# Kernel optimization log

Measured on AMD Instinct MI355X. Metric: run time of the kernel, lower is better.

The kernel has to match this reference:

```python
import jax, jax.numpy as jnp
import numpy as np

N0 = 16384; F_IN = 384; H = 512; E0 = 131072
DEPTH = 2; RATIO = 0.25; START_K = 6; K_INC = 1; INTERP_K = 6


def _pdist2(a, b):
    # squared euclidean distances [Na, Nb]
    d2 = jnp.sum(a * a, axis=1)[:, None] + jnp.sum(b * b, axis=1)[None, :] - 2.0 * (a @ b.T)
    return jnp.maximum(d2, 0.0)


def _fps(pos, n_keep):
    # farthest point sampling, deterministic start at node 0
    sel0 = jnp.zeros((n_keep,), jnp.int32)
    dist0 = jnp.sum((pos - pos[0]) ** 2, axis=-1)

    def body(i, st):
        sel, dist = st
        idx = jnp.argmax(dist).astype(jnp.int32)
        sel = sel.at[i].set(idx)
        dist = jnp.minimum(dist, jnp.sum((pos - pos[idx]) ** 2, axis=-1))
        return (sel, dist)

    sel, _ = jax.lax.fori_loop(1, n_keep, body, (sel0, dist0))
    return sel


def _knn_graph(pos, k):
    n = pos.shape[0]
    d2 = _pdist2(pos, pos)
    d2 = d2.at[jnp.arange(n), jnp.arange(n)].set(1e10)  # exclude self
    _, nbr = jax.lax.top_k(-d2, k)                      # [n, k] nearest neighbors
    src = nbr.reshape(-1)                               # flow: source_to_target
    dst = jnp.repeat(jnp.arange(n, dtype=nbr.dtype), k)
    return src, dst


def _gcn(x, src, dst, W, b):
    # GCNConv(improved=True): A_hat = D^-1/2 (A + 2I) D^-1/2, edge weights = 1
    n = x.shape[0]
    h = x @ W
    deg = jax.ops.segment_sum(jnp.ones(src.shape[0], x.dtype), dst, num_segments=n) + 2.0
    dinv = jax.lax.rsqrt(deg)
    coef = dinv[src] * dinv[dst]
    agg = jax.ops.segment_sum(h[src] * coef[:, None], dst, num_segments=n)
    agg = agg + h * (2.0 * dinv * dinv)[:, None]        # self loops with weight 2
    return agg + b


def _knn_interpolate(x, pos_x, pos_y, k):
    # interpolate coarse features x at pos_x onto fine positions pos_y (PyG knn_interpolate)
    d2 = _pdist2(pos_y, pos_x)                          # [Ny, Nx]
    negd, idx = jax.lax.top_k(-d2, k)                   # k nearest coarse points
    w = 1.0 / jnp.maximum(-negd, 1e-16)                 # [Ny, k]
    num = jnp.einsum('yk,ykf->yf', w, x[idx])
    return num / jnp.sum(w, axis=-1, keepdims=True)


def setup_inputs() -> dict:
    key = jax.random.key(0)
    ks = jax.random.split(key, 16)
    def w(k, fin, fout):
        return (jax.random.normal(k, (fin, fout), jnp.float32) / np.sqrt(fin)).astype(jnp.float32)
    return {
        'x': jax.random.normal(ks[0], (N0, F_IN), jnp.float32),
        'pos': jax.random.uniform(ks[1], (N0, 2), jnp.float32) * 100.0,
        'edge_index': jax.random.randint(ks[2], (2, E0), 0, N0, dtype=jnp.int32),
        'W_down0': w(ks[3], F_IN, H), 'b_down0': jnp.zeros((H,), jnp.float32),
        'W_down1': w(ks[4], H, H),   'b_down1': jnp.zeros((H,), jnp.float32),
        'W_up0': w(ks[5], H, H),     'b_up0': jnp.zeros((H,), jnp.float32),
        'W_up1': w(ks[6], H, H),     'b_up1': jnp.zeros((H,), jnp.float32),
        'W_lin': w(ks[7], H, H),     'b_lin': jnp.zeros((H,), jnp.float32),
    }


def reference(x, pos, edge_index, W_down0, b_down0, W_down1, b_down1,
              W_up0, b_up0, W_up1, b_up1, W_lin, b_lin):
    src, dst = edge_index[0], edge_index[1]
    Wd = [(W_down0, b_down0), (W_down1, b_down1)]
    Wu = [(W_up0, b_up0), (W_up1, b_up1)]
    all_pos = [pos]
    all_edges = [(src, dst)]
    for i in range(DEPTH):
        x = jax.nn.relu(_gcn(x, src, dst, *Wd[i]))
        n_keep = int(x.shape[0] * RATIO)
        perm = _fps(jax.lax.stop_gradient(pos), n_keep)
        pos = pos[perm]
        src, dst = _knn_graph(pos, START_K + i * K_INC)
        x = x[perm]
        all_pos.append(pos)
        all_edges.append((src, dst))
    for i in range(DEPTH):
        x = _knn_interpolate(x, all_pos[-i - 1], all_pos[-i - 2], INTERP_K)
        s, d = all_edges[-i - 2]
        x = jax.nn.relu(_gcn(x, s, d, *Wu[i]))
    return x @ W_lin + b_lin
```

## Files before the change

### kernel.cpp

```cpp
#include <hip/hip_runtime.h>

#define N0 16384
#define N1 4096
#define N2 1024
#define E0C 131072
#define FIN 384
#define HF 512

__device__ inline float4 f4fma(float w, const float4 v, float4 a) {
  a.x = fmaf(w, v.x, a.x); a.y = fmaf(w, v.y, a.y);
  a.z = fmaf(w, v.z, a.z); a.w = fmaf(w, v.w, a.w);
  return a;
}

__global__ __launch_bounds__(256)
void count_deg(const int* __restrict__ dst, int* __restrict__ cnt, int E) {
  int e = blockIdx.x * 256 + threadIdx.x;
  if (e < E) atomicAdd(&cnt[dst[e]], 1);
}

__global__ __launch_bounds__(1024)
void scan_offsets(const int* __restrict__ cnt, int* __restrict__ offs,
                  float* __restrict__ dinv) {
  __shared__ int ts[1024];
  const int t = threadIdx.x;
  int local[16];
  int sum = 0;
  #pragma unroll
  for (int j = 0; j < 16; ++j) { local[j] = cnt[t * 16 + j]; sum += local[j]; }
  ts[t] = sum;
  __syncthreads();
  for (int off = 1; off < 1024; off <<= 1) {
    int v = (t >= off) ? ts[t - off] : 0;
    __syncthreads();
    ts[t] += v;
    __syncthreads();
  }
  int run = ts[t] - sum;
  #pragma unroll
  for (int j = 0; j < 16; ++j) {
    offs[t * 16 + j] = run;
    dinv[t * 16 + j] = 1.0f / sqrtf((float)local[j] + 2.0f);
    run += local[j];
  }
  if (t == 1023) offs[N0] = run;
}

__global__ __launch_bounds__(256)
void fill_csr(const int* __restrict__ src, const int* __restrict__ dst,
              const int* __restrict__ offs, int* __restrict__ cursor,
              int* __restrict__ srcl, int E) {
  int e = blockIdx.x * 256 + threadIdx.x;
  if (e < E) {
    int d = dst[e];
    int p = atomicAdd(&cursor[d], 1);
    srcl[offs[d] + p] = src[e];
  }
}

template<int BM, int BN, int BK>
__global__ __launch_bounds__(256)
void gemm_f32(const float* __restrict__ A, const float* __restrict__ W,
              const float* __restrict__ bias, float* __restrict__ C,
              int M, int N, int K, int addBias) {
  __shared__ float As[BK][BM + 4];
  __shared__ float Ws[BK][BN];
  const int tid = threadIdx.x;
  const int bm = blockIdx.x * BM;
  const int bn = blockIdx.y * BN;
  const int tx = tid & 15;
  const int ty = tid >> 4;
  float acc[8][4];
  #pragma unroll
  for (int i = 0; i < 8; ++i)
    #pragma unroll
    for (int j = 0; j < 4; ++j) acc[i][j] = 0.f;

  for (int k0 = 0; k0 < K; k0 += BK) {
    #pragma unroll
    for (int h = 0; h < (BM * BK) / (256 * 4); ++h) {
      int q = tid + h * 256;
      int r = q >> 2;
      int c = (q & 3) << 2;
      float4 v = *(const float4*)(A + (size_t)(bm + r) * K + k0 + c);
      As[c][r] = v.x; As[c + 1][r] = v.y; As[c + 2][r] = v.z; As[c + 3][r] = v.w;
    }
    {
      int kk = tid >> 4;
      int n = (tid & 15) << 2;
      *(float4*)(&Ws[kk][n]) = *(const float4*)(W + (size_t)(k0 + kk) * N + bn + n);
    }
    __syncthreads();
    #pragma unroll
    for (int kk = 0; kk < BK; ++kk) {
      float4 b4 = *(const float4*)(&Ws[kk][tx << 2]);
      float4 a0 = *(const float4*)(&As[kk][ty << 3]);
      float4 a1 = *(const float4*)(&As[kk][(ty << 3) + 4]);
      float a[8] = {a0.x, a0.y, a0.z, a0.w, a1.x, a1.y, a1.z, a1.w};
      float b[4] = {b4.x, b4.y, b4.z, b4.w};
      #pragma unroll
      for (int i = 0; i < 8; ++i)
        #pragma unroll
        for (int j = 0; j < 4; ++j)
          acc[i][j] = fmaf(a[i], b[j], acc[i][j]);
    }
    __syncthreads();
  }
  #pragma unroll
  for (int i = 0; i < 8; ++i) {
    int row = bm + (ty << 3) + i;
    float4 o = {acc[i][0], acc[i][1], acc[i][2], acc[i][3]};
    if (addBias) {
      const float4 bb = *(const float4*)(bias + bn + (tx << 2));
      o.x += bb.x; o.y += bb.y; o.z += bb.z; o.w += bb.w;
    }
    *(float4*)(C + (size_t)row * N + bn + (tx << 2)) = o;
  }
}

__global__ __launch_bounds__(256)
void gcn_agg_csr(const float* __restrict__ h, const int* __restrict__ offs,
                 const int* __restrict__ srcl, const float* __restrict__ dinv,
                 const float* __restrict__ bias, float* __restrict__ out, int n) {
  const int wid = threadIdx.x >> 6, lane = threadIdx.x & 63;
  const int node = blockIdx.x * 4 + wid;
  if (node >= n) return;
  const float di = dinv[node];
  const int s0 = offs[node], s1 = offs[node + 1];
  float4 a0 = {0, 0, 0, 0}, a1 = {0, 0, 0, 0};
  for (int e = s0; e < s1; ++e) {
    const int s = srcl[e];
    const float w = dinv[s] * di;
    const float4* r = (const float4*)(h + (size_t)s * HF);
    a0 = f4fma(w, r[lane], a0);
    a1 = f4fma(w, r[64 + lane], a1);
  }
  const float sw = 2.0f * di * di;
  const float4* rs = (const float4*)(h + (size_t)node * HF);
  a0 = f4fma(sw, rs[lane], a0);
  a1 = f4fma(sw, rs[64 + lane], a1);
  const float4 b0 = *(const float4*)(bias + (lane << 2));
  const float4 b1 = *(const float4*)(bias + 256 + (lane << 2));
  a0.x = fmaxf(a0.x + b0.x, 0.f); a0.y = fmaxf(a0.y + b0.y, 0.f);
  a0.z = fmaxf(a0.z + b0.z, 0.f); a0.w = fmaxf(a0.w + b0.w, 0.f);
  a1.x = fmaxf(a1.x + b1.x, 0.f); a1.y = fmaxf(a1.y + b1.y, 0.f);
  a1.z = fmaxf(a1.z + b1.z, 0.f); a1.w = fmaxf(a1.w + b1.w, 0.f);
  float4* o = (float4*)(out + (size_t)node * HF);
  o[lane] = a0; o[64 + lane] = a1;
}

template<int K>
__global__ __launch_bounds__(256)
void gcn_agg_knn(const float* __restrict__ h, const int* __restrict__ nbr,
                 const float* __restrict__ bias, float* __restrict__ out, int n) {
  const int wid = threadIdx.x >> 6, lane = threadIdx.x & 63;
  const int node = blockIdx.x * 4 + wid;
  if (node >= n) return;
  const float di = 1.0f / sqrtf((float)(K + 2));
  const float w = di * di;
  float4 a0 = {0, 0, 0, 0}, a1 = {0, 0, 0, 0};
  #pragma unroll
  for (int j = 0; j < K; ++j) {
    const int s = nbr[node * K + j];
    const float4* r = (const float4*)(h + (size_t)s * HF);
    a0 = f4fma(w, r[lane], a0);
    a1 = f4fma(w, r[64 + lane], a1);
  }
  const float sw = 2.0f * di * di;
  const float4* rs = (const float4*)(h + (size_t)node * HF);
  a0 = f4fma(sw, rs[lane], a0);
  a1 = f4fma(sw, rs[64 + lane], a1);
  const float4 b0 = *(const float4*)(bias + (lane << 2));
  const float4 b1 = *(const float4*)(bias + 256 + (lane << 2));
  a0.x = fmaxf(a0.x + b0.x, 0.f); a0.y = fmaxf(a0.y + b0.y, 0.f);
  a0.z = fmaxf(a0.z + b0.z, 0.f); a0.w = fmaxf(a0.w + b0.w, 0.f);
  a1.x = fmaxf(a1.x + b1.x, 0.f); a1.y = fmaxf(a1.y + b1.y, 0.f);
  a1.z = fmaxf(a1.z + b1.z, 0.f); a1.w = fmaxf(a1.w + b1.w, 0.f);
  float4* o = (float4*)(out + (size_t)node * HF);
  o[lane] = a0; o[64 + lane] = a1;
}

__global__ __launch_bounds__(256)
void bin_hist(const float* __restrict__ pos, int* __restrict__ cid,
              int* __restrict__ hist, int n) {
  int i = blockIdx.x * 256 + threadIdx.x;
  if (i >= n) return;
  float x = pos[2 * i], y = pos[2 * i + 1];
  int cxi = (int)(x * 0.32f); cxi = cxi < 0 ? 0 : (cxi > 31 ? 31 : cxi);
  int cyi = (int)(y * 0.32f); cyi = cyi < 0 ? 0 : (cyi > 31 ? 31 : cyi);
  int c = cyi * 32 + cxi;
  cid[i] = c;
  atomicAdd(&hist[c], 1);
}

__global__ __launch_bounds__(1024)
void bin_scan(const int* __restrict__ hist, int* __restrict__ offs) {
  __shared__ int ts[1024];
  const int t = threadIdx.x;
  int v = hist[t];
  ts[t] = v;
  __syncthreads();
  for (int off = 1; off < 1024; off <<= 1) {
    int u = (t >= off) ? ts[t - off] : 0;
    __syncthreads();
    ts[t] += u;
    __syncthreads();
  }
  offs[t] = ts[t] - v;
  if (t == 1023) offs[1024] = ts[t];
}

__global__ __launch_bounds__(256)
void bin_scatter(const float* __restrict__ pos, const int* __restrict__ cid,
                 const int* __restrict__ offs, int* __restrict__ cursor,
                 float* __restrict__ sx, float* __restrict__ sy,
                 int* __restrict__ sid, int n) {
  int i = blockIdx.x * 256 + threadIdx.x;
  if (i >= n) return;
  int c = cid[i];
  int p = atomicAdd(&cursor[c], 1);
  int slot = offs[c] + p;
  sx[slot] = pos[2 * i];
  sy[slot] = pos[2 * i + 1];
  sid[slot] = i;
}

template<int NN>
__device__ __forceinline__ unsigned ror16(unsigned v) {
  return (unsigned)__builtin_amdgcn_update_dpp(0, (int)v, 0x120 | NN, 0xF, 0xF, false);
}

__device__ __forceinline__ void comb(unsigned& hi, unsigned& lo, float& x, float& y,
                                     unsigned ohi, unsigned olo, float ox, float oy) {
  unsigned long long a = ((unsigned long long)hi << 32) | lo;
  unsigned long long b = ((unsigned long long)ohi << 32) | olo;
  if (b > a) { hi = ohi; lo = olo; x = ox; y = oy; }
}

template<int N, int CHUNK, int NKEEP>
__global__ __launch_bounds__(1024)
void fps_pruned(const float* __restrict__ pos0,
                const float* __restrict__ sx, const float* __restrict__ sy,
                const int* __restrict__ sid,
                int* __restrict__ perm, float* __restrict__ pos_out) {
  const int t = threadIdx.x;
  const int base = t * CHUNK;
  float px[CHUNK], py[CHUNK], d[CHUNK];
  int id[CHUNK];
  float xmn = 3.4e38f, xmx = -3.4e38f, ymn = 3.4e38f, ymx = -3.4e38f;
  #pragma unroll
  for (int j = 0; j < CHUNK; ++j) {
    px[j] = sx[base + j]; py[j] = sy[base + j]; id[j] = sid[base + j];
    xmn = fminf(xmn, px[j]); xmx = fmaxf(xmx, px[j]);
    ymn = fminf(ymn, py[j]); ymx = fmaxf(ymx, py[j]);
  }
  float cx = pos0[0], cy = pos0[1];
  if (t == 0) { perm[0] = 0; pos_out[0] = cx; pos_out[1] = cy; }

  unsigned chi = 0, clo = 0; float ccx = 0.f, ccy = 0.f;
  {
    unsigned long long best = 0;
    #pragma unroll
    for (int j = 0; j < CHUNK; ++j) {
      float dx = __fsub_rn(px[j], cx), dy = __fsub_rn(py[j], cy);
      float nd = __fadd_rn(__fmul_rn(dx, dx), __fmul_rn(dy, dy));
      d[j] = nd;
      unsigned long long kv = ((unsigned long long)__float_as_uint(nd) << 32) |
                              (unsigned)(~(unsigned)id[j]);
      if (kv > best) { best = kv; ccx = px[j]; ccy = py[j]; }
    }
    chi = (unsigned)(best >> 32); clo = (unsigned)best;
  }
  float cmaxv = __uint_as_float(chi);

  __shared__ float4 e1[64];
  __shared__ float bc[2];

  for (int i = 1; i < NKEEP; ++i) {
    unsigned hi = chi, lo = clo; float wx = ccx, wy = ccy;
    {
      unsigned ohi, olo, ox, oy;
      ohi = ror16<1>(hi); olo = ror16<1>(lo); ox = ror16<1>(__float_as_uint(wx)); oy = ror16<1>(__float_as_uint(wy));
      comb(hi, lo, wx, wy, ohi, olo, __uint_as_float(ox), __uint_as_float(oy));
      ohi = ror16<2>(hi); olo = ror16<2>(lo); ox = ror16<2>(__float_as_uint(wx)); oy = ror16<2>(__float_as_uint(wy));
      comb(hi, lo, wx, wy, ohi, olo, __uint_as_float(ox), __uint_as_float(oy));
      ohi = ror16<4>(hi); olo = ror16<4>(lo); ox = ror16<4>(__float_as_uint(wx)); oy = ror16<4>(__float_as_uint(wy));
      comb(hi, lo, wx, wy, ohi, olo, __uint_as_float(ox), __uint_as_float(oy));
      ohi = ror16<8>(hi); olo = ror16<8>(lo); ox = ror16<8>(__float_as_uint(wx)); oy = ror16<8>(__float_as_uint(wy));
      comb(hi, lo, wx, wy, ohi, olo, __uint_as_float(ox), __uint_as_float(oy));
    }
    if ((t & 15) == 0)
      e1[t >> 4] = make_float4(__uint_as_float(hi), __uint_as_float(lo), wx, wy);
    __syncthreads();
    if (t < 16) {
      float4 a = e1[t];
      unsigned fhi = __float_as_uint(a.x), flo = __float_as_uint(a.y);
      float fx = a.z, fy = a.w;
      float4 b = e1[t + 16];
      comb(fhi, flo, fx, fy, __float_as_uint(b.x), __float_as_uint(b.y), b.z, b.w);
      b = e1[t + 32];
      comb(fhi, flo, fx, fy, __float_as_uint(b.x), __float_as_uint(b.y), b.z, b.w);
      b = e1[t + 48];
      comb(fhi, flo, fx, fy, __float_as_uint(b.x), __float_as_uint(b.y), b.z, b.w);
      unsigned ohi, olo, ox, oy;
      ohi = ror16<1>(fhi); olo = ror16<1>(flo); ox = ror16<1>(__float_as_uint(fx)); oy = ror16<1>(__float_as_uint(fy));
      comb(fhi, flo, fx, fy, ohi, olo, __uint_as_float(ox), __uint_as_float(oy));
      ohi = ror16<2>(fhi); olo = ror16<2>(flo); ox = ror16<2>(__float_as_uint(fx)); oy = ror16<2>(__float_as_uint(fy));
      comb(fhi, flo, fx, fy, ohi, olo, __uint_as_float(ox), __uint_as_float(oy));
      ohi = ror16<4>(fhi); olo = ror16<4>(flo); ox = ror16<4>(__float_as_uint(fx)); oy = ror16<4>(__float_as_uint(fy));
      comb(fhi, flo, fx, fy, ohi, olo, __uint_as_float(ox), __uint_as_float(oy));
      ohi = ror16<8>(fhi); olo = ror16<8>(flo); ox = ror16<8>(__float_as_uint(fx)); oy = ror16<8>(__float_as_uint(fy));
      comb(fhi, flo, fx, fy, ohi, olo, __uint_as_float(ox), __uint_as_float(oy));
      if (t == 0) {
        int idx = (int)(~flo);
        perm[i] = idx;
        pos_out[2 * i] = fx; pos_out[2 * i + 1] = fy;
        bc[0] = fx; bc[1] = fy;
      }
    }
    __syncthreads();
    cx = bc[0]; cy = bc[1];

    float mdx = fmaxf(fmaxf(__fsub_rn(xmn, cx), __fsub_rn(cx, xmx)), 0.f);
    float mdy = fmaxf(fmaxf(__fsub_rn(ymn, cy), __fsub_rn(cy, ymx)), 0.f);
    float mb = mdx * mdx + mdy * mdy;
    if (!(mb * 0.99999f > cmaxv)) {
      unsigned long long best = 0;
      float nccx = 0.f, nccy = 0.f;
      #pragma unroll
      for (int j = 0; j < CHUNK; ++j) {
        float dx = __fsub_rn(px[j], cx), dy = __fsub_rn(py[j], cy);
        float nd = __fadd_rn(__fmul_rn(dx, dx), __fmul_rn(dy, dy));
        float dn = fminf(d[j], nd);
        d[j] = dn;
        unsigned long long kv = ((unsigned long long)__float_as_uint(dn) << 32) |
                                (unsigned)(~(unsigned)id[j]);
        if (kv > best) { best = kv; nccx = px[j]; nccy = py[j]; }
      }
      chi = (unsigned)(best >> 32); clo = (unsigned)best;
      ccx = nccx; ccy = nccy;
      cmaxv = __uint_as_float(chi);
    }
  }
}

__global__ __launch_bounds__(256)
void gather_rows(const float* __restrict__ xin, const int* __restrict__ perm,
                 float* __restrict__ xout, int n) {
  const int wid = threadIdx.x >> 6, lane = threadIdx.x & 63;
  const int i = blockIdx.x * 4 + wid;
  if (i >= n) return;
  const int s = perm[i];
  const float4* r = (const float4*)(xin + (size_t)s * HF);
  float4* o = (float4*)(xout + (size_t)i * HF);
  o[lane] = r[lane];
  o[64 + lane] = r[64 + lane];
}

template<int NPTS, int K>
__global__ __launch_bounds__(256)
void knn_graph_kernel(const float* __restrict__ pos, int* __restrict__ srcout) {
  __shared__ float sx[NPTS], sy[NPTS], ss[NPTS];
  const int tid = threadIdx.x;
  for (int idx = tid; idx < NPTS; idx += 256) {
    float x = pos[2 * idx], y = pos[2 * idx + 1];
    sx[idx] = x; sy[idx] = y;
    ss[idx] = __fadd_rn(__fmul_rn(x, x), __fmul_rn(y, y));
  }
  __syncthreads();
  const int q = blockIdx.x * 256 + tid;
  const float qx = sx[q], qy = sy[q], qs = ss[q];
  float bd[K]; int bi[K];
  #pragma unroll
  for (int m = 0; m < K; ++m) { bd[m] = 3.4e38f; bi[m] = 0; }
  for (int j = 0; j < NPTS; ++j) {
    if (j == q) continue;
    float dot = __fadd_rn(__fmul_rn(qx, sx[j]), __fmul_rn(qy, sy[j]));
    float d2 = fmaxf(__fsub_rn(__fadd_rn(qs, ss[j]), __fmul_rn(2.0f, dot)), 0.0f);
    if (d2 < bd[K - 1]) {
      bool pr[K];
      #pragma unroll
      for (int m = 0; m < K; ++m) pr[m] = (d2 < bd[m]);
      #pragma unroll
      for (int m = K - 1; m >= 1; --m) {
        bd[m] = pr[m] ? (pr[m - 1] ? bd[m - 1] : d2) : bd[m];
        bi[m] = pr[m] ? (pr[m - 1] ? bi[m - 1] : j) : bi[m];
      }
      if (pr[0]) { bd[0] = d2; bi[0] = j; }
    }
  }
  #pragma unroll
  for (int m = 0; m < K; ++m) srcout[q * K + m] = bi[m];
}

template<int NX, int K>
__global__ __launch_bounds__(256)
void interp_topk(const float* __restrict__ posy, const float* __restrict__ posx,
                 int* __restrict__ oidx, float* __restrict__ ow,
                 float* __restrict__ owsum) {
  __shared__ float sx[NX], sy[NX], ss[NX];
  const int tid = threadIdx.x;
  for (int idx = tid; idx < NX; idx += 256) {
    float x = posx[2 * idx], y = posx[2 * idx + 1];
    sx[idx] = x; sy[idx] = y;
    ss[idx] = __fadd_rn(__fmul_rn(x, x), __fmul_rn(y, y));
  }
  __syncthreads();
  const int q = blockIdx.x * 256 + tid;
  const float qx = posy[2 * q], qy = posy[2 * q + 1];
  const float qs = __fadd_rn(__fmul_rn(qx, qx), __fmul_rn(qy, qy));
  float bd[K]; int bi[K];
  #pragma unroll
  for (int m = 0; m < K; ++m) { bd[m] = 3.4e38f; bi[m] = 0; }
  for (int j = 0; j < NX; ++j) {
    float dot = __fadd_rn(__fmul_rn(qx, sx[j]), __fmul_rn(qy, sy[j]));
    float d2 = fmaxf(__fsub_rn(__fadd_rn(qs, ss[j]), __fmul_rn(2.0f, dot)), 0.0f);
    if (d2 < bd[K - 1]) {
      bool pr[K];
      #pragma unroll
      for (int m = 0; m < K; ++m) pr[m] = (d2 < bd[m]);
      #pragma unroll
      for (int m = K - 1; m >= 1; --m) {
        bd[m] = pr[m] ? (pr[m - 1] ? bd[m - 1] : d2) : bd[m];
        bi[m] = pr[m] ? (pr[m - 1] ? bi[m - 1] : j) : bi[m];
      }
      if (pr[0]) { bd[0] = d2; bi[0] = j; }
    }
  }
  float wsum = 0.f;
  #pragma unroll
  for (int m = 0; m < K; ++m) {
    float w = 1.0f / fmaxf(bd[m], 1e-16f);
    ow[q * K + m] = w;
    oidx[q * K + m] = bi[m];
    wsum = __fadd_rn(wsum, w);
  }
  owsum[q] = wsum;
}

template<int K>
__global__ __launch_bounds__(256)
void interp_combine(const float* __restrict__ xin, const int* __restrict__ idx,
                    const float* __restrict__ w, const float* __restrict__ wsum,
                    float* __restrict__ out, int ny) {
  const int wid = threadIdx.x >> 6, lane = threadIdx.x & 63;
  const int q = blockIdx.x * 4 + wid;
  if (q >= ny) return;
  float4 a0 = {0, 0, 0, 0}, a1 = {0, 0, 0, 0};
  #pragma unroll
  for (int m = 0; m < K; ++m) {
    const int s = idx[q * K + m];
    const float wk = w[q * K + m];
    const float4* r = (const float4*)(xin + (size_t)s * HF);
    a0 = f4fma(wk, r[lane], a0);
    a1 = f4fma(wk, r[64 + lane], a1);
  }
  const float inv = wsum[q];
  a0.x /= inv; a0.y /= inv; a0.z /= inv; a0.w /= inv;
  a1.x /= inv; a1.y /= inv; a1.z /= inv; a1.w /= inv;
  float4* o = (float4*)(out + (size_t)q * HF);
  o[lane] = a0; o[64 + lane] = a1;
}

extern "C" void kernel_launch(void* const* d_in, const int* in_sizes, int n_in,
                              void* d_out, int out_size, void* d_ws, size_t ws_size,
                              hipStream_t stream) {
  const float* x    = (const float*)d_in[0];
  const float* pos  = (const float*)d_in[1];
  const int*   ei   = (const int*)d_in[2];
  const float* Wd0  = (const float*)d_in[3];
  const float* bd0  = (const float*)d_in[4];
  const float* Wd1  = (const float*)d_in[5];
  const float* bd1  = (const float*)d_in[6];
  const float* Wu0  = (const float*)d_in[7];
  const float* bu0  = (const float*)d_in[8];
  const float* Wu1  = (const float*)d_in[9];
  const float* bu1  = (const float*)d_in[10];
  const float* Wl   = (const float*)d_in[11];
  const float* bl   = (const float*)d_in[12];
  float* out = (float*)d_out;

  char* ws = (char*)d_ws;
  size_t off = 0;
  auto alloc = [&](size_t bytes) -> char* {
    char* p = ws + off;
    off = (off + bytes + 255) & ~(size_t)255;
    return p;
  };
  float* bufA   = (float*)alloc((size_t)N0 * HF * 4);
  float* bufB   = (float*)alloc((size_t)N0 * HF * 4);
  float* bufC   = (float*)alloc((size_t)N1 * HF * 4);
  float* x2     = (float*)alloc((size_t)N2 * HF * 4);
  int*   offs0  = (int*)alloc((N0 + 1) * 4);
  int*   srcl0  = (int*)alloc(E0C * 4);
  int*   cnt    = (int*)alloc(N0 * 4);
  int*   cursor = (int*)alloc(N0 * 4);
  float* dinv0  = (float*)alloc(N0 * 4);
  int*   perm0  = (int*)alloc(N1 * 4);
  float* pos1   = (float*)alloc(N1 * 2 * 4);
  int*   src1   = (int*)alloc(N1 * 6 * 4);
  int*   perm1  = (int*)alloc(N2 * 4);
  float* pos2   = (float*)alloc(N2 * 2 * 4);
  int*   iidx   = (int*)alloc((size_t)N0 * 6 * 4);
  float* iw     = (float*)alloc((size_t)N0 * 6 * 4);
  float* iwsum  = (float*)alloc(N0 * 4);
  float* bsx    = (float*)alloc(N0 * 4);
  float* bsy    = (float*)alloc(N0 * 4);
  int*   bsid   = (int*)alloc(N0 * 4);
  int*   bcid   = (int*)alloc(N0 * 4);
  int*   bhist  = (int*)alloc(1024 * 4);
  int*   bcur   = (int*)alloc(1024 * 4);
  int*   boffs  = (int*)alloc(1025 * 4);

  float* h1   = bufB;
  float* x1f  = bufB + (size_t)N1 * HF;
  float* hu0  = bufB;
  float* xu0f = bufB + (size_t)N1 * HF;

  hipMemsetAsync(cnt, 0, N0 * 4, stream);
  hipMemsetAsync(cursor, 0, N0 * 4, stream);
  count_deg<<<E0C / 256, 256, 0, stream>>>(ei + E0C, cnt, E0C);
  scan_offsets<<<1, 1024, 0, stream>>>(cnt, offs0, dinv0);
  fill_csr<<<E0C / 256, 256, 0, stream>>>(ei, ei + E0C, offs0, cursor, srcl0, E0C);

  hipMemsetAsync(bhist, 0, 1024 * 4, stream);
  hipMemsetAsync(bcur, 0, 1024 * 4, stream);
  bin_hist<<<N0 / 256, 256, 0, stream>>>(pos, bcid, bhist, N0);
  bin_scan<<<1, 1024, 0, stream>>>(bhist, boffs);
  bin_scatter<<<N0 / 256, 256, 0, stream>>>(pos, bcid, boffs, bcur, bsx, bsy, bsid, N0);

  gemm_f32<128, 64, 16><<<dim3(N0 / 128, HF / 64), 256, 0, stream>>>(
      x, Wd0, nullptr, bufA, N0, HF, FIN, 0);
  gcn_agg_csr<<<N0 / 4, 256, 0, stream>>>(bufA, offs0, srcl0, dinv0, bd0, bufB, N0);
  fps_pruned<N0, 16, N1><<<1, 1024, 0, stream>>>(pos, bsx, bsy, bsid, perm0, pos1);
  gather_rows<<<N1 / 4, 256, 0, stream>>>(bufB, perm0, bufC, N1);
  knn_graph_kernel<N1, 6><<<N1 / 256, 256, 0, stream>>>(pos1, src1);

  hipMemsetAsync(bhist, 0, 1024 * 4, stream);
  hipMemsetAsync(bcur, 0, 1024 * 4, stream);
  bin_hist<<<N1 / 256, 256, 0, stream>>>(pos1, bcid, bhist, N1);
  bin_scan<<<1, 1024, 0, stream>>>(bhist, boffs);
  bin_scatter<<<N1 / 256, 256, 0, stream>>>(pos1, bcid, boffs, bcur, bsx, bsy, bsid, N1);

  gemm_f32<128, 64, 16><<<dim3(N1 / 128, HF / 64), 256, 0, stream>>>(
      bufC, Wd1, nullptr, h1, N1, HF, HF, 0);
  gcn_agg_knn<6><<<N1 / 4, 256, 0, stream>>>(h1, src1, bd1, x1f, N1);
  fps_pruned<N1, 4, N2><<<1, 1024, 0, stream>>>(pos1, bsx, bsy, bsid, perm1, pos2);
  gather_rows<<<N2 / 4, 256, 0, stream>>>(x1f, perm1, x2, N2);

  interp_topk<N2, 6><<<N1 / 256, 256, 0, stream>>>(pos1, pos2, iidx, iw, iwsum);
  interp_combine<6><<<N1 / 4, 256, 0, stream>>>(x2, iidx, iw, iwsum, bufC, N1);
  gemm_f32<128, 64, 16><<<dim3(N1 / 128, HF / 64), 256, 0, stream>>>(
      bufC, Wu0, nullptr, hu0, N1, HF, HF, 0);
  gcn_agg_knn<6><<<N1 / 4, 256, 0, stream>>>(hu0, src1, bu0, xu0f, N1);

  interp_topk<N1, 6><<<N0 / 256, 256, 0, stream>>>(pos, pos1, iidx, iw, iwsum);
  interp_combine<6><<<N0 / 4, 256, 0, stream>>>(xu0f, iidx, iw, iwsum, bufA, N0);
  gemm_f32<128, 64, 16><<<dim3(N0 / 128, HF / 64), 256, 0, stream>>>(
      bufA, Wu1, nullptr, bufB, N0, HF, HF, 0);
  gcn_agg_csr<<<N0 / 4, 256, 0, stream>>>(bufB, offs0, srcl0, dinv0, bu1, bufA, N0);

  gemm_f32<128, 64, 16><<<dim3(N0 / 128, HF / 64), 256, 0, stream>>>(
      bufA, Wl, bl, out, N0, HF, HF, 1);
}
```

Baseline: 9.219 ms.

## Restructure FPS argmax reduction to single-wave pass with positions in LDS

Rewrites the farthest-point-sampling kernel so each thread publishes its chunk's best key to shared memory. A single wave then reduces all candidates with a strided scan, DPP row rotations and readlanes, instead of every thread running a DPP reduction followed by a second cross-row stage. Point coordinates move from registers into shared memory to lower register pressure. The second FPS level now runs with 256 threads instead of 1024. This trims per-iteration reduction work on the serial critical path, at the cost of a shared-memory read per point in the distance update and a serial scan over 16 candidates per lane in the 1024-thread case.

```diff
diff --git a/kernel.cpp b/kernel.cpp
--- a/kernel.cpp
+++ b/kernel.cpp
@@ -230,92 +230,95 @@
   return (unsigned)__builtin_amdgcn_update_dpp(0, (int)v, 0x120 | NN, 0xF, 0xF, false);
 }
 
-__device__ __forceinline__ void comb(unsigned& hi, unsigned& lo, float& x, float& y,
-                                     unsigned ohi, unsigned olo, float ox, float oy) {
-  unsigned long long a = ((unsigned long long)hi << 32) | lo;
-  unsigned long long b = ((unsigned long long)ohi << 32) | olo;
-  if (b > a) { hi = ohi; lo = olo; x = ox; y = oy; }
-}
-
-template<int N, int CHUNK, int NKEEP>
-__global__ __launch_bounds__(1024)
-void fps_pruned(const float* __restrict__ pos0,
-                const float* __restrict__ sx, const float* __restrict__ sy,
-                const int* __restrict__ sid,
-                int* __restrict__ perm, float* __restrict__ pos_out) {
+template<int N, int NCH, int NKEEP>
+__global__ __launch_bounds__(NCH)
+void fps_fast(const float* __restrict__ pos0,
+              const float* __restrict__ sx, const float* __restrict__ sy,
+              const int* __restrict__ sid,
+              int* __restrict__ perm, float* __restrict__ pos_out) {
+  constexpr int CHUNK = N / NCH;
   const int t = threadIdx.x;
   const int base = t * CHUNK;
-  float px[CHUNK], py[CHUNK], d[CHUNK];
-  int id[CHUNK];
+
+  __shared__ float pxl[N];
+  __shared__ float pyl[N];
+  __shared__ unsigned long long ck[NCH];
+  __shared__ float2 cp[NCH];
+  __shared__ float bc[2];
+
+  float d[CHUNK];
+  unsigned kid[CHUNK];
   float xmn = 3.4e38f, xmx = -3.4e38f, ymn = 3.4e38f, ymx = -3.4e38f;
-  #pragma unroll
-  for (int j = 0; j < CHUNK; ++j) {
-    px[j] = sx[base + j]; py[j] = sy[base + j]; id[j] = sid[base + j];
-    xmn = fminf(xmn, px[j]); xmx = fmaxf(xmx, px[j]);
-    ymn = fminf(ymn, py[j]); ymx = fmaxf(ymx, py[j]);
-  }
+
   float cx = pos0[0], cy = pos0[1];
   if (t == 0) { perm[0] = 0; pos_out[0] = cx; pos_out[1] = cy; }
 
-  unsigned chi = 0, clo = 0; float ccx = 0.f, ccy = 0.f;
   {
-    unsigned long long best = 0;
+    unsigned long long best = 0; float bx = 0.f, by = 0.f;
     #pragma unroll
     for (int j = 0; j < CHUNK; ++j) {
-      float dx = __fsub_rn(px[j], cx), dy = __fsub_rn(py[j], cy);
+      float qx = sx[base + j], qy = sy[base + j];
+      kid[j] = ~(unsigned)sid[base + j];
+      pxl[j * NCH + t] = qx;
+      pyl[j * NCH + t] = qy;
+      xmn = fminf(xmn, qx); xmx = fmaxf(xmx, qx);
+      ymn = fminf(ymn, qy); ymx = fmaxf(ymx, qy);
+      float dx = __fsub_rn(qx, cx), dy = __fsub_rn(qy, cy);
       float nd = __fadd_rn(__fmul_rn(dx, dx), __fmul_rn(dy, dy));
       d[j] = nd;
-      unsigned long long kv = ((unsigned long long)__float_as_uint(nd) << 32) |
-                              (unsigned)(~(unsigned)id[j]);
-      if (kv > best) { best = kv; ccx = px[j]; ccy = py[j]; }
-    }
-    chi = (unsigned)(best >> 32); clo = (unsigned)best;
-  }
-  float cmaxv = __uint_as_float(chi);
-
-  __shared__ float4 e1[64];
-  __shared__ float bc[2];
+      unsigned long long kv =
+          ((unsigned long long)__float_as_uint(nd) << 32) | kid[j];
+      if (kv > best) { best = kv; bx = qx; by = qy; }
+    }
+    ck[t] = best;
+    cp[t] = make_float2(bx, by);
+  }
+  float cmax = __uint_as_float((unsigned)(ck[t] >> 32));
+  __syncthreads();
 
   for (int i = 1; i < NKEEP; ++i) {
-    unsigned hi = chi, lo = clo; float wx = ccx, wy = ccy;
-    {
-      unsigned ohi, olo, ox, oy;
-      ohi = ror16<1>(hi); olo = ror16<1>(lo); ox = ror16<1>(__float_as_uint(wx)); oy = ror16<1>(__float_as_uint(wy));
-      comb(hi, lo, wx, wy, ohi, olo, __uint_as_float(ox), __uint_as_float(oy));
-      ohi = ror16<2>(hi); olo = ror16<2>(lo); ox = ror16<2>(__float_as_uint(wx)); oy = ror16<2>(__float_as_uint(wy));
-      comb(hi, lo, wx, wy, ohi, olo, __uint_as_float(ox), __uint_as_float(oy));
-      ohi = ror16<4>(hi); olo = ror16<4>(lo); ox = ror16<4>(__float_as_uint(wx)); oy = ror16<4>(__float_as_uint(wy));
-      comb(hi, lo, wx, wy, ohi, olo, __uint_as_float(ox), __uint_as_float(oy));
-      ohi = ror16<8>(hi); olo = ror16<8>(lo); ox = ror16<8>(__float_as_uint(wx)); oy = ror16<8>(__float_as_uint(wy));
-      comb(hi, lo, wx, wy, ohi, olo, __uint_as_float(ox), __uint_as_float(oy));
-    }
-    if ((t & 15) == 0)
-      e1[t >> 4] = make_float4(__uint_as_float(hi), __uint_as_float(lo), wx, wy);
-    __syncthreads();
-    if (t < 16) {
-      float4 a = e1[t];
-      unsigned fhi = __float_as_uint(a.x), flo = __float_as_uint(a.y);
-      float fx = a.z, fy = a.w;
-      float4 b = e1[t + 16];
-      comb(fhi, flo, fx, fy, __float_as_uint(b.x), __float_as_uint(b.y), b.z, b.w);
-      b = e1[t + 32];
-      comb(fhi, flo, fx, fy, __float_as_uint(b.x), __float_as_uint(b.y), b.z, b.w);
-      b = e1[t + 48];
-      comb(fhi, flo, fx, fy, __float_as_uint(b.x), __float_as_uint(b.y), b.z, b.w);
-      unsigned ohi, olo, ox, oy;
-      ohi = ror16<1>(fhi); olo = ror16<1>(flo); ox = ror16<1>(__float_as_uint(fx)); oy = ror16<1>(__float_as_uint(fy));
-      comb(fhi, flo, fx, fy, ohi, olo, __uint_as_float(ox), __uint_as_float(oy));
-      ohi = ror16<2>(fhi); olo = ror16<2>(flo); ox = ror16<2>(__float_as_uint(fx)); oy = ror16<2>(__float_as_uint(fy));
-      comb(fhi, flo, fx, fy, ohi, olo, __uint_as_float(ox), __uint_as_float(oy));
-      ohi = ror16<4>(fhi); olo = ror16<4>(flo); ox = ror16<4>(__float_as_uint(fx)); oy = ror16<4>(__float_as_uint(fy));
-      comb(fhi, flo, fx, fy, ohi, olo, __uint_as_float(ox), __uint_as_float(oy));
-      ohi = ror16<8>(fhi); olo = ror16<8>(flo); ox = ror16<8>(__float_as_uint(fx)); oy = ror16<8>(__float_as_uint(fy));
-      comb(fhi, flo, fx, fy, ohi, olo, __uint_as_float(ox), __uint_as_float(oy));
+    if (t < 64) {
+      unsigned long long bk = 0;
+      int sl = 0;
+      #pragma unroll
+      for (int j = 0; j < NCH / 64; ++j) {
+        unsigned long long k = ck[t + j * 64];
+        if (k > bk) { bk = k; sl = t + j * 64; }
+      }
+      {
+        unsigned hi, lo, ohi, olo; int os;
+        hi = (unsigned)(bk >> 32); lo = (unsigned)bk;
+        ohi = ror16<1>(hi); olo = ror16<1>(lo); os = (int)ror16<1>((unsigned)sl);
+        { unsigned long long ok = ((unsigned long long)ohi << 32) | olo;
+          if (ok > bk) { bk = ok; sl = os; } }
+        hi = (unsigned)(bk >> 32); lo = (unsigned)bk;
+        ohi = ror16<2>(hi); olo = ror16<2>(lo); os = (int)ror16<2>((unsigned)sl);
+        { unsigned long long ok = ((unsigned long long)ohi << 32) | olo;
+          if (ok > bk) { bk = ok; sl = os; } }
+        hi = (unsigned)(bk >> 32); lo = (unsigned)bk;
+        ohi = ror16<4>(hi); olo = ror16<4>(lo); os = (int)ror16<4>((unsigned)sl);
+        { unsigned long long ok = ((unsigned long long)ohi << 32) | olo;
+          if (ok > bk) { bk = ok; sl = os; } }
+        hi = (unsigned)(bk >> 32); lo = (unsigned)bk;
+        ohi = ror16<8>(hi); olo = ror16<8>(lo); os = (int)ror16<8>((unsigned)sl);
+        { unsigned long long ok = ((unsigned long long)ohi << 32) | olo;
+          if (ok > bk) { bk = ok; sl = os; } }
+      }
+      unsigned hi = (unsigned)(bk >> 32), lo = (unsigned)bk;
+      unsigned long long fb = 0; int fs = 0;
+      #pragma unroll
+      for (int r = 0; r < 4; ++r) {
+        unsigned h = (unsigned)__builtin_amdgcn_readlane((int)hi, r * 16);
+        unsigned l = (unsigned)__builtin_amdgcn_readlane((int)lo, r * 16);
+        int s = __builtin_amdgcn_readlane(sl, r * 16);
+        unsigned long long k = ((unsigned long long)h << 32) | l;
+        if (k > fb) { fb = k; fs = s; }
+      }
       if (t == 0) {
-        int idx = (int)(~flo);
-        perm[i] = idx;
-        pos_out[2 * i] = fx; pos_out[2 * i + 1] = fy;
-        bc[0] = fx; bc[1] = fy;
+        float2 c = cp[fs];
+        perm[i] = (int)(~(unsigned)fb);
+        pos_out[2 * i] = c.x; pos_out[2 * i + 1] = c.y;
+        bc[0] = c.x; bc[1] = c.y;
       }
     }
     __syncthreads();
@@ -324,23 +327,24 @@
     float mdx = fmaxf(fmaxf(__fsub_rn(xmn, cx), __fsub_rn(cx, xmx)), 0.f);
     float mdy = fmaxf(fmaxf(__fsub_rn(ymn, cy), __fsub_rn(cy, ymx)), 0.f);
     float mb = mdx * mdx + mdy * mdy;
-    if (!(mb * 0.99999f > cmaxv)) {
-      unsigned long long best = 0;
-      float nccx = 0.f, nccy = 0.f;
+    if (!(mb * 0.99999f > cmax)) {
+      unsigned long long best = 0; float bx = 0.f, by = 0.f;
       #pragma unroll
       for (int j = 0; j < CHUNK; ++j) {
-        float dx = __fsub_rn(px[j], cx), dy = __fsub_rn(py[j], cy);
+        float qx = pxl[j * NCH + t], qy = pyl[j * NCH + t];
+        float dx = __fsub_rn(qx, cx), dy = __fsub_rn(qy, cy);
         float nd = __fadd_rn(__fmul_rn(dx, dx), __fmul_rn(dy, dy));
         float dn = fminf(d[j], nd);
         d[j] = dn;
-        unsigned long long kv = ((unsigned long long)__float_as_uint(dn) << 32) |
-                                (unsigned)(~(unsigned)id[j]);
-        if (kv > best) { best = kv; nccx = px[j]; nccy = py[j]; }
-      }
-      chi = (unsigned)(best >> 32); clo = (unsigned)best;
-      ccx = nccx; ccy = nccy;
-      cmaxv = __uint_as_float(chi);
-    }
+        unsigned long long kv =
+            ((unsigned long long)__float_as_uint(dn) << 32) | kid[j];
+        if (kv > best) { best = kv; bx = qx; by = qy; }
+      }
+      ck[t] = best;
+      cp[t] = make_float2(bx, by);
+      cmax = __uint_as_float((unsigned)(best >> 32));
+    }
+    __syncthreads();
   }
 }
 
@@ -532,7 +536,7 @@
   gemm_f32<128, 64, 16><<<dim3(N0 / 128, HF / 64), 256, 0, stream>>>(
       x, Wd0, nullptr, bufA, N0, HF, FIN, 0);
   gcn_agg_csr<<<N0 / 4, 256, 0, stream>>>(bufA, offs0, srcl0, dinv0, bd0, bufB, N0);
-  fps_pruned<N0, 16, N1><<<1, 1024, 0, stream>>>(pos, bsx, bsy, bsid, perm0, pos1);
+  fps_fast<N0, 1024, N1><<<1, 1024, 0, stream>>>(pos, bsx, bsy, bsid, perm0, pos1);
   gather_rows<<<N1 / 4, 256, 0, stream>>>(bufB, perm0, bufC, N1);
   knn_graph_kernel<N1, 6><<<N1 / 256, 256, 0, stream>>>(pos1, src1);
 
@@ -545,7 +549,7 @@
   gemm_f32<128, 64, 16><<<dim3(N1 / 128, HF / 64), 256, 0, stream>>>(
       bufC, Wd1, nullptr, h1, N1, HF, HF, 0);
   gcn_agg_knn<6><<<N1 / 4, 256, 0, stream>>>(h1, src1, bd1, x1f, N1);
-  fps_pruned<N1, 4, N2><<<1, 1024, 0, stream>>>(pos1, bsx, bsy, bsid, perm1, pos2);
+  fps_fast<N1, 256, N2><<<1, 256, 0, stream>>>(pos1, bsx, bsy, bsid, perm1, pos2);
   gather_rows<<<N2 / 4, 256, 0, stream>>>(x1f, perm1, x2, N2);
 
   interp_topk<N2, 6><<<N1 / 256, 256, 0, stream>>>(pos1, pos2, iidx, iw, iwsum);
```

After: 8.045 ms. 1.15x faster.
